# Performance work log

Hardware: AMD Instinct MI355X
Metric: run time of the kernel (lower is better)

## Reference

```python
import jax, jax.numpy as jnp
import numpy as np

N = 20000   # nodes
E = 240000  # edges (avg degree 12)
D = 128     # hidden_dim
H = 4       # heads
C = D // H  # head dim = 32
L = 3       # layers


def _ln(x, g, b):
    m = x.mean(-1, keepdims=True)
    v = ((x - m) ** 2).mean(-1, keepdims=True)
    return (x - m) / jnp.sqrt(v + 1e-5) * g + b


def setup_inputs() -> dict:
    key = jax.random.key(0)
    ks = iter(jax.random.split(key, 64))
    def w(shape, s=0.02):
        return jax.random.normal(next(ks), shape, jnp.float32) * s
    z = lambda shape: jnp.zeros(shape, jnp.float32)
    o = lambda shape: jnp.ones(shape, jnp.float32)
    inp = {
        'xyz': jax.random.normal(next(ks), (N, 3), jnp.float32) * 10.0,
        'attr': jax.random.uniform(next(ks), (N, 1), jnp.float32),
        'edge_index': jax.random.randint(next(ks), (2, E), 0, N, jnp.int32),
        # input encoder
        'enc_W': w((4, D)), 'enc_b': z((D,)), 'enc_g': o((D,)), 'enc_bb': z((D,)),
        # relative position MLP
        'pos_W1': w((3, D)), 'pos_b1': z((D,)), 'pos_g': o((D,)), 'pos_bb': z((D,)),
        'pos_W2': w((D, D)), 'pos_b2': z((D,)),
        # TransformerConv per-layer params (stacked over L)
        'Wq': w((L, D, D)), 'bq': z((L, D)),
        'Wk': w((L, D, D)), 'bk': z((L, D)),
        'Wv': w((L, D, D)), 'bv': z((L, D)),
        'We': w((L, D, D)),                 # lin_edge (no bias in PyG)
        'Wskip': w((L, D, D)), 'bskip': z((L, D)),
        'Wbeta': w((L, 3 * D, 1)),          # lin_beta (no bias)
        'ln1_g': o((L, D)), 'ln1_b': z((L, D)),
        'ln2_g': o((L, D)), 'ln2_b': z((L, D)),
        'fW1': w((L, D, 2 * D)), 'fb1': z((L, 2 * D)),
        'fW2': w((L, 2 * D, D)), 'fb2': z((L, D)),
        # heads
        'cls_W1': w((D, D // 2)), 'cls_b1': z((D // 2,)),
        'cls_W2': w((D // 2, 4)), 'cls_b2': z((4,)),
        'box_W1': w((D, D // 2)), 'box_b1': z((D // 2,)),
        'box_W2': w((D // 2, 7)), 'box_b2': z((7,)),
    }
    return inp


def reference(xyz, attr, edge_index, enc_W, enc_b, enc_g, enc_bb,
              pos_W1, pos_b1, pos_g, pos_bb, pos_W2, pos_b2,
              Wq, bq, Wk, bk, Wv, bv, We, Wskip, bskip, Wbeta,
              ln1_g, ln1_b, ln2_g, ln2_b, fW1, fb1, fW2, fb2,
              cls_W1, cls_b1, cls_W2, cls_b2, box_W1, box_b1, box_W2, box_b2):
    n = xyz.shape[0]
    src, dst = edge_index[0], edge_index[1]  # x_j = x[src], x_i = x[dst]; aggregate at dst
    inv_sqrt_c = 1.0 / float(np.sqrt(C))

    # input encoder: Linear -> LayerNorm -> ReLU
    x = jnp.concatenate([xyz, attr], axis=-1)
    x = jax.nn.relu(_ln(x @ enc_W + enc_b, enc_g, enc_bb))

    # relative position encoding per edge: i, j = edge_index; rel = xyz[j] - xyz[i]
    rel = xyz[dst] - xyz[src]
    e = jax.nn.relu(_ln(rel @ pos_W1 + pos_b1, pos_g, pos_bb)) @ pos_W2 + pos_b2  # [E, D]

    for l in range(L):
        # TransformerConv (beta=True, concat=True, edge_dim=D), eval mode (no dropout)
        q = (x @ Wq[l] + bq[l]).reshape(n, H, C)
        k = (x @ Wk[l] + bk[l]).reshape(n, H, C)
        v = (x @ Wv[l] + bv[l]).reshape(n, H, C)
        ee = (e @ We[l]).reshape(-1, H, C)          # [E, H, C]
        kj = k[src] + ee                             # edge-conditioned keys
        alpha = (q[dst] * kj).sum(-1) * inv_sqrt_c   # [E, H]
        amax = jax.ops.segment_max(alpha, dst, num_segments=n)
        ex = jnp.exp(alpha - amax[dst])
        den = jax.ops.segment_sum(ex, dst, num_segments=n)
        a = ex / den[dst]                            # scatter softmax over in-edges of dst
        msg = (v[src] + ee) * a[:, :, None]
        out = jax.ops.segment_sum(msg, dst, num_segments=n).reshape(n, D)
        # beta-gated skip
        r = x @ Wskip[l] + bskip[l]
        beta = jax.nn.sigmoid(jnp.concatenate([out, r, out - r], axis=-1) @ Wbeta[l])  # [N,1]
        out = beta * r + (1.0 - beta) * out
        # residual + LN + FFN + residual + LN
        x = _ln(out + x, ln1_g[l], ln1_b[l])
        h = jax.nn.gelu(x @ fW1[l] + fb1[l], approximate=False) @ fW2[l] + fb2[l]
        x = _ln(h + x, ln2_g[l], ln2_b[l])

    cls_logits = jax.nn.relu(x @ cls_W1 + cls_b1) @ cls_W2 + cls_b2  # [N, 4]
    box_pred = jax.nn.relu(x @ box_W1 + box_b1) @ box_W2 + box_b2    # [N, 7]
    return (cls_logits, box_pred)
```

## Files before the change

kernel.cpp:

```cpp
#include <hip/hip_runtime.h>
#include <hip/hip_bf16.h>
#include <math.h>

#define DD 128

typedef __attribute__((ext_vector_type(8))) short short8;
typedef __attribute__((ext_vector_type(4))) float f32x4;


__device__ __forceinline__ unsigned short f2b(float f) {
    unsigned u = __float_as_uint(f);
    return (unsigned short)((u + 0x7FFFu + ((u >> 16) & 1u)) >> 16);
}
__device__ __forceinline__ float b2f(unsigned short b) {
    return __uint_as_float(((unsigned)b) << 16);
}
__device__ __forceinline__ unsigned packbf(float a, float b) {
    return (unsigned)f2b(a) | ((unsigned)f2b(b) << 16);
}

__device__ __forceinline__ void redsum2_128(float& a, float& b) {
    #pragma unroll
    for (int off = 32; off > 0; off >>= 1) {
        a += __shfl_down(a, off);
        b += __shfl_down(b, off);
    }
    __shared__ float sa[2], sb[2];
    int w = threadIdx.x >> 6;
    if ((threadIdx.x & 63) == 0) { sa[w] = a; sb[w] = b; }
    __syncthreads();
    a = sa[0] + sa[1];
    b = sb[0] + sb[1];
    __syncthreads();
}


__global__ void packw12_kernel(const float* __restrict__ Wq, const float* __restrict__ Wk,
                               const float* __restrict__ Wv, const float* __restrict__ Ws,
                               unsigned* __restrict__ Wp) {
    int bid = blockIdx.x, y = blockIdx.y, d = threadIdx.x;
    int l = y >> 2, wt = y & 3;
    const float* W = (wt == 0 ? Wq : wt == 1 ? Wk : wt == 2 ? Wv : Ws) + (size_t)l * DD * DD;
    float w0 = W[(size_t)(2 * bid) * DD + d];
    float w1 = W[(size_t)(2 * bid + 1) * DD + d];
    Wp[y * 8192 + (((d << 6) + bid) ^ ((d & 7) << 2))] = packbf(w0, w1);
}

__global__ void wcombp_kernel(const float* __restrict__ W2, const float* __restrict__ b2,
                              const float* __restrict__ We, unsigned* __restrict__ Wp,
                              float* __restrict__ b2We) {
    int bid = blockIdx.x, y = blockIdx.y, d = threadIdx.x;
    const float* We_l = We + (size_t)y * DD * DD;
    __shared__ float sa0[DD], sa1[DD];
    if (bid < 64) { sa0[d] = W2[(2 * bid) * DD + d]; sa1[d] = W2[(2 * bid + 1) * DD + d]; }
    else          { sa0[d] = b2[d]; sa1[d] = 0.f; }
    __syncthreads();
    float acc0 = 0.f, acc1 = 0.f;
    #pragma unroll 8
    for (int kk = 0; kk < DD; ++kk) {
        float w = We_l[kk * DD + d];
        acc0 += sa0[kk] * w;
        acc1 += sa1[kk] * w;
    }
    if (bid < 64) Wp[y * 8192 + (((d << 6) + bid) ^ ((d & 7) << 2))] = packbf(acc0, acc1);
    else          b2We[y * DD + d] = acc0;
}

struct B4 { const float* b[4]; };

__global__ __launch_bounds__(256) void proj_kernel(
        const unsigned short* __restrict__ xb, const unsigned* __restrict__ Wp4, B4 bias,
        unsigned short* __restrict__ qkv, float* __restrict__ rbuf, int rowsN, int rtN,
        const float4* __restrict__ rel4, const float* __restrict__ pw,
        const float* __restrict__ bbp, const unsigned* __restrict__ Wpee,
        const float* __restrict__ biasee, unsigned short* __restrict__ eeout,
        int rowsE, int rtE) {
    __shared__ unsigned Bt[8192];
    __shared__ float sc[640];
    const int t = threadIdx.x;
    const int lane = t & 63, wid = t >> 6;
    const int kqo = (lane >> 4) * 8;

    if ((int)blockIdx.x < rtE) {
        const int rowBase = (int)blockIdx.x << 6;
        #pragma unroll
        for (int i = 0; i < 8; ++i)
            *(uint4*)&Bt[(i * 256 + t) * 4] = *(const uint4*)&Wpee[(i * 256 + t) * 4];
        for (int i = t; i < 640; i += 256)
            sc[i] = (i < 512) ? pw[i] : bbp[i - 512];
        int arow = rowBase + wid * 16 + (lane & 15);
        if (arow > rowsE - 1) arow = rowsE - 1;
        float4 rv = rel4[arow];
        __syncthreads();
        short8 a[4];
        #pragma unroll
        for (int kc = 0; kc < 4; ++kc) {
            union { short8 s; unsigned short u[8]; } cv;
            #pragma unroll
            for (int j = 0; j < 8; ++j) {
                int d = kc * 32 + kqo + j;
                float y = fmaf(rv.x, sc[d], fmaf(rv.y, sc[128 + d], fmaf(rv.z, sc[256 + d], sc[384 + d])));
                cv.u[j] = f2b(fmaxf(fmaf(y, rv.w, sc[512 + d]), 0.f));
            }
            a[kc] = cv.s;
        }
        f32x4 acc[8];
        #pragma unroll
        for (int i = 0; i < 8; ++i) acc[i] = (f32x4){0.f, 0.f, 0.f, 0.f};
        #pragma unroll
        for (int ng = 0; ng < 8; ++ng) {
            int col = ng * 16 + (lane & 15);
            #pragma unroll
            for (int kc = 0; kc < 4; ++kc) {
                int kidx = kc * 16 + (lane >> 4) * 4;
                const short8 b = *(const short8*)((const char*)Bt +
                        ((((col << 6) + kidx) ^ ((col & 7) << 2)) << 2));
                acc[ng] = __builtin_amdgcn_mfma_f32_16x16x32_bf16(a[kc], b, acc[ng], 0, 0, 0);
            }
        }
        __syncthreads();
        unsigned short* sb16 = (unsigned short*)Bt;
        #pragma unroll
        for (int ng = 0; ng < 8; ++ng) {
            int col = ng * 16 + (lane & 15);
            float bv = biasee[col];
            int cp = col >> 1, cb = col & 1;
            #pragma unroll
            for (int r = 0; r < 4; ++r) {
                int row = wid * 16 + (lane >> 4) * 4 + r;
                sb16[((row << 6) + (cp ^ ((row & 7) << 2))) * 2 + cb] = f2b(acc[ng][r] + bv);
            }
        }
        __syncthreads();
        unsigned* outw = (unsigned*)eeout;
        #pragma unroll
        for (int i = 0; i < 4; ++i) {
            int j = i * 1024 + t * 4;
            int row = j >> 6, cp = j & 63;
            uint4 v = *(const uint4*)&Bt[(row << 6) + (cp ^ ((row & 7) << 2))];
            int grow = rowBase + row;
            if (grow < rowsE) *(uint4*)&outw[(size_t)grow * 64 + cp] = v;
        }
    } else {
        int bidx = (int)blockIdx.x - rtE;
        const int y = bidx / rtN;
        const int rowBase = (bidx % rtN) << 6;
        const unsigned* Wp = Wp4 + y * 8192;
        #pragma unroll
        for (int i = 0; i < 8; ++i)
            *(uint4*)&Bt[(i * 256 + t) * 4] = *(const uint4*)&Wp[(i * 256 + t) * 4];
        int arow = rowBase + wid * 16 + (lane & 15);
        if (arow > rowsN - 1) arow = rowsN - 1;
        short8 a[4];
        #pragma unroll
        for (int kc = 0; kc < 4; ++kc)
            a[kc] = *(const short8*)(xb + (size_t)arow * DD + kc * 32 + kqo);
        __syncthreads();
        f32x4 acc[8];
        #pragma unroll
        for (int i = 0; i < 8; ++i) acc[i] = (f32x4){0.f, 0.f, 0.f, 0.f};
        #pragma unroll
        for (int ng = 0; ng < 8; ++ng) {
            int col = ng * 16 + (lane & 15);
            #pragma unroll
            for (int kc = 0; kc < 4; ++kc) {
                int kidx = kc * 16 + (lane >> 4) * 4;
                const short8 b = *(const short8*)((const char*)Bt +
                        ((((col << 6) + kidx) ^ ((col & 7) << 2)) << 2));
                acc[ng] = __builtin_amdgcn_mfma_f32_16x16x32_bf16(a[kc], b, acc[ng], 0, 0, 0);
            }
        }
        const float* bs = bias.b[y];
        if (y == 3) {
            #pragma unroll
            for (int ng = 0; ng < 8; ++ng) {
                int col = ng * 16 + (lane & 15);
                float bv = bs[col];
                #pragma unroll
                for (int r = 0; r < 4; ++r) {
                    int grow = rowBase + wid * 16 + (lane >> 4) * 4 + r;
                    if (grow < rowsN) rbuf[(size_t)grow * DD + col] = acc[ng][r] + bv;
                }
            }
            return;
        }
        __syncthreads();
        unsigned short* sb16 = (unsigned short*)Bt;
        #pragma unroll
        for (int ng = 0; ng < 8; ++ng) {
            int col = ng * 16 + (lane & 15);
            float bv = bs[col];
            int cp = col >> 1, cb = col & 1;
            #pragma unroll
            for (int r = 0; r < 4; ++r) {
                int row = wid * 16 + (lane >> 4) * 4 + r;
                sb16[((row << 6) + (cp ^ ((row & 7) << 2))) * 2 + cb] = f2b(acc[ng][r] + bv);
            }
        }
        __syncthreads();
        unsigned* outw = (unsigned*)qkv;
        #pragma unroll
        for (int i = 0; i < 4; ++i) {
            int j = i * 1024 + t * 4;
            int row = j >> 6, cp = j & 63;
            uint4 v = *(const uint4*)&Bt[(row << 6) + (cp ^ ((row & 7) << 2))];
            int grow = rowBase + row;
            if (grow < rowsN) *(uint4*)&outw[(size_t)grow * 192 + (y << 6) + cp] = v;
        }
    }
}

template <int ACT>
__global__ __launch_bounds__(256) void mgemm(
        const unsigned short* __restrict__ A, const float* __restrict__ W,
        const float* __restrict__ bias, unsigned short* __restrict__ out,
        int rows, int K, int Dout) {
    __shared__ unsigned Bt[8192];
    const int t = threadIdx.x;
    const int rowBase = blockIdx.x << 6;
    const int colBase = blockIdx.y << 7;
    const int lane = t & 63, wid = t >> 6;
    f32x4 acc[8];
    #pragma unroll
    for (int i = 0; i < 8; ++i) acc[i] = (f32x4){0.f, 0.f, 0.f, 0.f};
    int arow = rowBase + wid * 16 + (lane & 15);
    if (arow > rows - 1) arow = rows - 1;
    const int kqo = (lane >> 4) * 8;
    for (int k0 = 0; k0 < K; k0 += 128) {
        if (k0) __syncthreads();
        #pragma unroll 8
        for (int it = 0; it < 32; ++it) {
            int idx = it * 256 + t;
            int n = idx & 127, kp = idx >> 7;
            int krow = k0 + kp * 2;
            float w0 = W[(size_t)krow * Dout + colBase + n];
            float w1 = W[(size_t)(krow + 1) * Dout + colBase + n];
            Bt[((n << 6) + kp) ^ ((n & 7) << 2)] = packbf(w0, w1);
        }
        __syncthreads();
        short8 a[4];
        #pragma unroll
        for (int kc = 0; kc < 4; ++kc)
            a[kc] = *(const short8*)(A + (size_t)arow * K + k0 + kc * 32 + kqo);
        #pragma unroll
        for (int ng = 0; ng < 8; ++ng) {
            int col = ng * 16 + (lane & 15);
            #pragma unroll
            for (int kc = 0; kc < 4; ++kc) {
                int kidx = kc * 16 + (lane >> 4) * 4;
                const short8 b = *(const short8*)((const char*)Bt +
                        ((((col << 6) + kidx) ^ ((col & 7) << 2)) << 2));
                acc[ng] = __builtin_amdgcn_mfma_f32_16x16x32_bf16(a[kc], b, acc[ng], 0, 0, 0);
            }
        }
    }
    __syncthreads();
    unsigned short* sb16 = (unsigned short*)Bt;
    #pragma unroll
    for (int ng = 0; ng < 8; ++ng) {
        int col = ng * 16 + (lane & 15);
        float bv = bias[colBase + col];
        int cp = col >> 1, cb = col & 1;
        #pragma unroll
        for (int r = 0; r < 4; ++r) {
            int row = wid * 16 + (lane >> 4) * 4 + r;
            float val = acc[ng][r] + bv;
            if (ACT == 1) val = 0.5f * val * (1.f + erff(val * 0.70710678118654752f));
            else if (ACT == 2) val = fmaxf(val, 0.f);
            sb16[((row << 6) + (cp ^ ((row & 7) << 2))) * 2 + cb] = f2b(val);
        }
    }
    __syncthreads();
    unsigned* outw = (unsigned*)out;
    const int strideU = Dout >> 1, cbU = colBase >> 1;
    #pragma unroll
    for (int i = 0; i < 4; ++i) {
        int j = i * 1024 + t * 4;
        int row = j >> 6, cp = j & 63;
        uint4 v = *(const uint4*)&Bt[(row << 6) + (cp ^ ((row & 7) << 2))];
        int grow = rowBase + row;
        if (grow < rows) *(uint4*)&outw[(size_t)grow * strideU + cbU + cp] = v;
    }
}

__global__ __launch_bounds__(256) void ffn_fused(
        const unsigned short* __restrict__ xbin, const float* __restrict__ W1,
        const float* __restrict__ b1f, const float* __restrict__ W2,
        const float* __restrict__ b2f, const float* __restrict__ g,
        const float* __restrict__ bbn, float* __restrict__ x,
        unsigned short* __restrict__ xb, int rows) {
    __shared__ unsigned Bt[8192];
    __shared__ unsigned h1t[8192];
    const int t = threadIdx.x;
    const int rowBase = blockIdx.x << 6;
    const int lane = t & 63, wid = t >> 6;
    const int kqo = (lane >> 4) * 8;
    int arow = rowBase + wid * 16 + (lane & 15);
    if (arow > rows - 1) arow = rows - 1;

    short8 a[4];
    #pragma unroll
    for (int kc = 0; kc < 4; ++kc)
        a[kc] = *(const short8*)(xbin + (size_t)arow * DD + kc * 32 + kqo);

    unsigned short* h16 = (unsigned short*)h1t;
    for (int half = 0; half < 2; ++half) {
        if (half) __syncthreads();
        #pragma unroll 8
        for (int it = 0; it < 32; ++it) {
            int idx = it * 256 + t;
            int n = idx & 127, kp = idx >> 7;
            float w0 = W1[(size_t)(2 * kp) * 256 + half * 128 + n];
            float w1 = W1[(size_t)(2 * kp + 1) * 256 + half * 128 + n];
            Bt[((n << 6) + kp) ^ ((n & 7) << 2)] = packbf(w0, w1);
        }
        __syncthreads();
        f32x4 acc[8];
        #pragma unroll
        for (int i = 0; i < 8; ++i) acc[i] = (f32x4){0.f, 0.f, 0.f, 0.f};
        #pragma unroll
        for (int ng = 0; ng < 8; ++ng) {
            int col = ng * 16 + (lane & 15);
            #pragma unroll
            for (int kc = 0; kc < 4; ++kc) {
                int kidx = kc * 16 + (lane >> 4) * 4;
                const short8 b = *(const short8*)((const char*)Bt +
                        ((((col << 6) + kidx) ^ ((col & 7) << 2)) << 2));
                acc[ng] = __builtin_amdgcn_mfma_f32_16x16x32_bf16(a[kc], b, acc[ng], 0, 0, 0);
            }
        }
        #pragma unroll
        for (int ng = 0; ng < 8; ++ng) {
            int col = half * 128 + ng * 16 + (lane & 15);
            float bv = b1f[col];
            int cp = col >> 1, cb = col & 1;
            #pragma unroll
            for (int r = 0; r < 4; ++r) {
                int row = wid * 16 + (lane >> 4) * 4 + r;
                float val = acc[ng][r] + bv;
                val = 0.5f * val * (1.f + erff(val * 0.70710678118654752f));
                h16[((row << 7) + (cp ^ ((row & 7) << 2))) * 2 + cb] = f2b(val);
            }
        }
    }
    f32x4 accF[8];
    #pragma unroll
    for (int i = 0; i < 8; ++i) accF[i] = (f32x4){0.f, 0.f, 0.f, 0.f};
    const int lrow = wid * 16 + (lane & 15);
    for (int c = 0; c < 2; ++c) {
        __syncthreads();
        #pragma unroll 8
        for (int it = 0; it < 32; ++it) {
            int idx = it * 256 + t;
            int n = idx & 127, kp = idx >> 7;
            int krow = c * 128 + kp * 2;
            float w0 = W2[(size_t)krow * DD + n];
            float w1 = W2[(size_t)(krow + 1) * DD + n];
            Bt[((n << 6) + kp) ^ ((n & 7) << 2)] = packbf(w0, w1);
        }
        __syncthreads();
        short8 ah[4];
        #pragma unroll
        for (int kc = 0; kc < 4; ++kc) {
            int cp4 = c * 64 + kc * 16 + (lane >> 4) * 4;
            ah[kc] = *(const short8*)&h1t[(lrow << 7) + (cp4 ^ ((lrow & 7) << 2))];
        }
        #pragma unroll
        for (int ng = 0; ng < 8; ++ng) {
            int col = ng * 16 + (lane & 15);
            #pragma unroll
            for (int kc = 0; kc < 4; ++kc) {
                int kidx = kc * 16 + (lane >> 4) * 4;
                const short8 b = *(const short8*)((const char*)Bt +
                        ((((col << 6) + kidx) ^ ((col & 7) << 2)) << 2));
                accF[ng] = __builtin_amdgcn_mfma_f32_16x16x32_bf16(ah[kc], b, accF[ng], 0, 0, 0);
            }
        }
    }
    float tt[8][4];
    float rs[4] = {0.f, 0.f, 0.f, 0.f}, rs2[4] = {0.f, 0.f, 0.f, 0.f};
    #pragma unroll
    for (int ng = 0; ng < 8; ++ng) {
        int col = ng * 16 + (lane & 15);
        float bv = b2f[col];
        #pragma unroll
        for (int r = 0; r < 4; ++r) {
            int grow = rowBase + wid * 16 + (lane >> 4) * 4 + r;
            float xo = (grow < rows) ? x[(size_t)grow * DD + col] : 0.f;
            float v = accF[ng][r] + bv + xo;
            tt[ng][r] = v;
            rs[r] += v;
            rs2[r] += v * v;
        }
    }
    #pragma unroll
    for (int r = 0; r < 4; ++r) {
        #pragma unroll
        for (int m = 1; m < 16; m <<= 1) {
            rs[r] += __shfl_xor(rs[r], m);
            rs2[r] += __shfl_xor(rs2[r], m);
        }
    }
    __syncthreads();
    unsigned short* sb16 = (unsigned short*)Bt;
    #pragma unroll
    for (int ng = 0; ng < 8; ++ng) {
        int col = ng * 16 + (lane & 15);
        float gg = g[col], bbb = bbn[col];
        int cp = col >> 1, cb = col & 1;
        #pragma unroll
        for (int r = 0; r < 4; ++r) {
            int grow = rowBase + wid * 16 + (lane >> 4) * 4 + r;
            float mean = rs[r] * (1.f / DD);
            float var = rs2[r] * (1.f / DD) - mean * mean;
            float val = (tt[ng][r] - mean) * rsqrtf(var + 1e-5f) * gg + bbb;
            if (grow < rows) x[(size_t)grow * DD + col] = val;
            int row = wid * 16 + (lane >> 4) * 4 + r;
            sb16[((row << 6) + (cp ^ ((row & 7) << 2))) * 2 + cb] = f2b(val);
        }
    }
    __syncthreads();
    unsigned* outw = (unsigned*)xb;
    #pragma unroll
    for (int i = 0; i < 4; ++i) {
        int j = i * 1024 + t * 4;
        int row = j >> 6, cp = j & 63;
        uint4 v = *(const uint4*)&Bt[(row << 6) + (cp ^ ((row & 7) << 2))];
        int grow = rowBase + row;
        if (grow < rows) *(uint4*)&outw[(size_t)grow * 64 + cp] = v;
    }
}


__global__ void enc_kernel(const float* __restrict__ xyz, const float* __restrict__ attr,
                           const float* __restrict__ W, const float* __restrict__ b,
                           const float* __restrict__ g, const float* __restrict__ bb,
                           float* __restrict__ x, unsigned short* __restrict__ xb) {
    int i = blockIdx.x, d = threadIdx.x;
    __shared__ float sin4[4];
    if (d < 3) sin4[d] = xyz[i * 3 + d];
    if (d == 3) sin4[3] = attr[i];
    __syncthreads();
    float y = b[d];
    #pragma unroll
    for (int kk = 0; kk < 4; ++kk) y += sin4[kk] * W[kk * DD + d];
    float s = y, s2 = y * y;
    redsum2_128(s, s2);
    float mean = s * (1.0f / DD);
    float var = s2 * (1.0f / DD) - mean * mean;
    float xn = fmaxf((y - mean) * rsqrtf(var + 1e-5f) * g[d] + bb[d], 0.f);
    x[i * DD + d] = xn;
    xb[(size_t)i * DD + d] = f2b(xn);
}

__global__ void posprep_kernel(const float* __restrict__ W1, const float* __restrict__ b1,
                               const float* __restrict__ g, float* __restrict__ pw) {
    int d = threadIdx.x;
    float w0 = W1[d], w1 = W1[DD + d], w2 = W1[2 * DD + d], b = b1[d];
    float s0 = w0, s1 = w1;
    redsum2_128(s0, s1);
    float s2 = w2, s3 = b;
    redsum2_128(s2, s3);
    float c0 = w0 - s0 * (1.f / DD), c1 = w1 - s1 * (1.f / DD);
    float c2 = w2 - s2 * (1.f / DD), bc = b - s3 * (1.f / DD);
    float gd = g[d];
    pw[d] = c0 * gd; pw[DD + d] = c1 * gd; pw[2 * DD + d] = c2 * gd; pw[3 * DD + d] = bc * gd;
    float p0 = c0 * c0, p1 = c0 * c1; redsum2_128(p0, p1);
    float p2 = c0 * c2, p3 = c1 * c1; redsum2_128(p2, p3);
    float p4 = c1 * c2, p5 = c2 * c2; redsum2_128(p4, p5);
    float p6 = c0 * bc, p7 = c1 * bc; redsum2_128(p6, p7);
    float p8 = c2 * bc, p9 = bc * bc; redsum2_128(p8, p9);
    if (d == 0) {
        pw[512] = p0 * (1.f / DD); pw[513] = p1 * (1.f / DD); pw[514] = p2 * (1.f / DD);
        pw[515] = p3 * (1.f / DD); pw[516] = p4 * (1.f / DD); pw[517] = p5 * (1.f / DD);
        pw[518] = p6 * (1.f / DD); pw[519] = p7 * (1.f / DD); pw[520] = p8 * (1.f / DD);
        pw[521] = p9 * (1.f / DD);
    }
}


__global__ void hist_kernel(const int* __restrict__ ei, int* __restrict__ deg, int E) {
    int e = blockIdx.x * blockDim.x + threadIdx.x;
    if (e < E) atomicAdd(&deg[ei[E + e]], 1);
}

__global__ void scan_kernel(const int* __restrict__ deg, int* __restrict__ ptr, int n) {
    __shared__ int partial[1024];
    int t = threadIdx.x;
    int CH = (n + 1023) >> 10;
    int beg = t * CH;
    int end = beg + CH; if (end > n) end = n;
    int s = 0;
    for (int i = beg; i < end; ++i) s += deg[i];
    partial[t] = s;
    __syncthreads();
    for (int off = 1; off < 1024; off <<= 1) {
        int add = (t >= off) ? partial[t - off] : 0;
        __syncthreads();
        partial[t] += add;
        __syncthreads();
    }
    int base = (t == 0) ? 0 : partial[t - 1];
    for (int i = beg; i < end; ++i) {
        ptr[i] = base;
        base += deg[i];
    }
    if (end == n && beg < n) ptr[n] = base;
}

__global__ void scatter_kernel(const int* __restrict__ ei, const float* __restrict__ xyz,
                               const float* __restrict__ pw, const int* __restrict__ ptr,
                               int* __restrict__ cur, int* __restrict__ cs_src,
                               float4* __restrict__ rel4, int E) {
    int e = blockIdx.x * blockDim.x + threadIdx.x;
    if (e >= E) return;
    int srcn = ei[e], dstn = ei[E + e];
    int p = atomicAdd(&cur[dstn], 1);
    int slot = ptr[dstn] + p;
    cs_src[slot] = srcn;
    float r0 = xyz[dstn * 3]     - xyz[srcn * 3];
    float r1 = xyz[dstn * 3 + 1] - xyz[srcn * 3 + 1];
    float r2 = xyz[dstn * 3 + 2] - xyz[srcn * 3 + 2];
    float var = pw[512] * r0 * r0 + pw[515] * r1 * r1 + pw[517] * r2 * r2
              + 2.f * (pw[513] * r0 * r1 + pw[514] * r0 * r2 + pw[516] * r1 * r2)
              + 2.f * (pw[518] * r0 + pw[519] * r1 + pw[520] * r2) + pw[521];
    rel4[slot] = make_float4(r0, r1, r2, rsqrtf(var + 1e-5f));
}

__global__ __launch_bounds__(256) void aggc_kernel(
        const unsigned* __restrict__ qkv, const unsigned* __restrict__ ee,
        const int* __restrict__ ptr, const int* __restrict__ cs_src,
        const float* __restrict__ r, const float* __restrict__ Wb,
        const float* __restrict__ g1, const float* __restrict__ b1,
        float* __restrict__ x, unsigned* __restrict__ xbw, int N) {
    const int wave = threadIdx.x >> 6;
    const int lane = threadIdx.x & 63;
    const int node = ((int)blockIdx.x << 1) + (wave >> 1);
    const int half = wave & 1;
    __shared__ float sS[4];
    __shared__ float sA0[4][64];
    __shared__ float sA1[4][64];

    float s = 0.f, a0 = 0.f, a1 = 0.f;
    float q0 = 0.f, q1 = 0.f;
    int beg = 0, end = 0;
    if (node < N) {
        unsigned qp = qkv[(size_t)node * 192 + lane];
        q0 = b2f((unsigned short)qp);
        q1 = b2f((unsigned short)(qp >> 16));
        beg = ptr[node];
        end = ptr[node + 1];
    }
    int idx = beg + half;
    unsigned epN = 0, kpN = 0, vpN = 0;
    if (idx < end) {
        int j = cs_src[idx];
        epN = __builtin_nontemporal_load(&ee[(size_t)idx * 64 + lane]);
        kpN = qkv[(size_t)j * 192 + 64 + lane];
        vpN = qkv[(size_t)j * 192 + 128 + lane];
    }
    for (; idx < end; idx += 2) {
        unsigned ep = epN, kp = kpN, vp = vpN;
        int nidx = idx + 2;
        if (nidx < end) {
            int jn = cs_src[nidx];
            epN = __builtin_nontemporal_load(&ee[(size_t)nidx * 64 + lane]);
            kpN = qkv[(size_t)jn * 192 + 64 + lane];
            vpN = qkv[(size_t)jn * 192 + 128 + lane];
        }
        float e0 = b2f((unsigned short)ep), e1 = b2f((unsigned short)(ep >> 16));
        float kj0 = b2f((unsigned short)kp) + e0;
        float kj1 = b2f((unsigned short)(kp >> 16)) + e1;
        float p = q0 * kj0 + q1 * kj1;
        p += __shfl_xor(p, 1); p += __shfl_xor(p, 2);
        p += __shfl_xor(p, 4); p += __shfl_xor(p, 8);
        float w = __expf(p * 0.17677669529663687f);
        s += w;
        a0 += (b2f((unsigned short)vp) + e0) * w;
        a1 += (b2f((unsigned short)(vp >> 16)) + e1) * w;
    }
    sS[wave] = s;
    sA0[wave][lane] = a0;
    sA1[wave][lane] = a1;
    __syncthreads();
    if (half != 0 || node >= N) return;
    s  = sS[wave] + sS[wave + 1];
    a0 = sA0[wave][lane] + sA0[wave + 1][lane];
    a1 = sA1[wave][lane] + sA1[wave + 1][lane];

    float inv_s = (s > 0.f) ? 1.f / s : 0.f;
    float od0 = a0 * inv_s, od1 = a1 * inv_s;
    float2 rd = *(const float2*)&r[(size_t)node * DD + lane * 2];
    float2 wb0 = *(const float2*)&Wb[lane * 2];
    float2 wb1 = *(const float2*)&Wb[DD + lane * 2];
    float2 wb2 = *(const float2*)&Wb[2 * DD + lane * 2];
    float part = od0 * wb0.x + rd.x * wb1.x + (od0 - rd.x) * wb2.x
               + od1 * wb0.y + rd.y * wb1.y + (od1 - rd.y) * wb2.y;
    #pragma unroll
    for (int m = 1; m < 64; m <<= 1) part += __shfl_xor(part, m);
    float beta = 1.f / (1.f + __expf(-part));
    float2 xo = *(const float2*)&x[(size_t)node * DD + lane * 2];
    float t0 = beta * rd.x + (1.f - beta) * od0 + xo.x;
    float t1 = beta * rd.y + (1.f - beta) * od1 + xo.y;
    float ss = t0 + t1, ss2 = t0 * t0 + t1 * t1;
    #pragma unroll
    for (int m = 1; m < 64; m <<= 1) { ss += __shfl_xor(ss, m); ss2 += __shfl_xor(ss2, m); }
    float mean = ss * (1.f / DD);
    float var = ss2 * (1.f / DD) - mean * mean;
    float inv = rsqrtf(var + 1e-5f);
    float2 gg = *(const float2*)&g1[lane * 2];
    float2 bbv = *(const float2*)&b1[lane * 2];
    float2 res;
    res.x = (t0 - mean) * inv * gg.x + bbv.x;
    res.y = (t1 - mean) * inv * gg.y + bbv.y;
    *(float2*)&x[(size_t)node * DD + lane * 2] = res;
    xbw[(size_t)node * 64 + lane] = packbf(res.x, res.y);
}


__global__ void headprep_kernel(const float* __restrict__ cW1, const float* __restrict__ cb1,
                                const float* __restrict__ bW1, const float* __restrict__ bb1,
                                float* __restrict__ W1cat, float* __restrict__ b1cat) {
    int kk = blockIdx.x, d = threadIdx.x;
    W1cat[kk * DD + d] = (d < 64) ? cW1[kk * 64 + d] : bW1[kk * 64 + (d - 64)];
    if (kk == 0) b1cat[d] = (d < 64) ? cb1[d] : bb1[d - 64];
}

__global__ __launch_bounds__(256) void heads2_kernel(
        const unsigned* __restrict__ hh, const float* __restrict__ cW2,
        const float* __restrict__ cb2, const float* __restrict__ bW2,
        const float* __restrict__ bb2, float* __restrict__ outc,
        float* __restrict__ outb, int N) {
    int node = (blockIdx.x << 2) + (threadIdx.x >> 6);
    if (node >= N) return;
    const int lane = threadIdx.x & 63;
    unsigned hp = hh[(size_t)node * 64 + lane];
    float h0 = b2f((unsigned short)hp), h1 = b2f((unsigned short)(hp >> 16));
    bool isCls = lane < 32;
    int dd = isCls ? 2 * lane : 2 * lane - 128 + 64;
    float c[4], bx[7];
    #pragma unroll
    for (int j = 0; j < 4; ++j)
        c[j] = isCls ? h0 * cW2[dd * 4 + j] + h1 * cW2[(dd + 1) * 4 + j] : 0.f;
    #pragma unroll
    for (int j = 0; j < 7; ++j)
        bx[j] = isCls ? 0.f : h0 * bW2[dd * 7 + j] + h1 * bW2[(dd + 1) * 7 + j];
    #pragma unroll
    for (int m = 1; m < 32; m <<= 1) {
        #pragma unroll
        for (int j = 0; j < 4; ++j) c[j] += __shfl_xor(c[j], m);
        #pragma unroll
        for (int j = 0; j < 7; ++j) bx[j] += __shfl_xor(bx[j], m);
    }
    if (lane == 0) {
        #pragma unroll
        for (int j = 0; j < 4; ++j) outc[(size_t)node * 4 + j] = c[j] + cb2[j];
    } else if (lane == 32) {
        #pragma unroll
        for (int j = 0; j < 7; ++j) outb[(size_t)node * 7 + j] = bx[j] + bb2[j];
    }
}

extern "C" void kernel_launch(void* const* d_in, const int* in_sizes, int n_in,
                              void* d_out, int out_size, void* d_ws, size_t ws_size,
                              hipStream_t stream) {
    const float* xyz   = (const float*)d_in[0];
    const float* attr  = (const float*)d_in[1];
    const int*   ei    = (const int*)d_in[2];
    const float* encW  = (const float*)d_in[3];
    const float* encb  = (const float*)d_in[4];
    const float* encg  = (const float*)d_in[5];
    const float* encbb = (const float*)d_in[6];
    const float* posW1 = (const float*)d_in[7];
    const float* posb1 = (const float*)d_in[8];
    const float* posg  = (const float*)d_in[9];
    const float* posbb = (const float*)d_in[10];
    const float* posW2 = (const float*)d_in[11];
    const float* posb2 = (const float*)d_in[12];
    const float* Wq    = (const float*)d_in[13];
    const float* bq    = (const float*)d_in[14];
    const float* Wk    = (const float*)d_in[15];
    const float* bk    = (const float*)d_in[16];
    const float* Wv    = (const float*)d_in[17];
    const float* bv    = (const float*)d_in[18];
    const float* We    = (const float*)d_in[19];
    const float* Wskip = (const float*)d_in[20];
    const float* bskip = (const float*)d_in[21];
    const float* Wbeta = (const float*)d_in[22];
    const float* ln1g  = (const float*)d_in[23];
    const float* ln1b  = (const float*)d_in[24];
    const float* ln2g  = (const float*)d_in[25];
    const float* ln2b  = (const float*)d_in[26];
    const float* fW1   = (const float*)d_in[27];
    const float* fb1   = (const float*)d_in[28];
    const float* fW2   = (const float*)d_in[29];
    const float* fb2   = (const float*)d_in[30];
    const float* cW1   = (const float*)d_in[31];
    const float* cb1   = (const float*)d_in[32];
    const float* cW2   = (const float*)d_in[33];
    const float* cb2   = (const float*)d_in[34];
    const float* bW1   = (const float*)d_in[35];
    const float* bb1   = (const float*)d_in[36];
    const float* bW2   = (const float*)d_in[37];
    const float* bb2   = (const float*)d_in[38];

    const int N = in_sizes[0] / 3;
    const int E = in_sizes[2] / 2;

    size_t off = 0;
    auto alloc = [&](size_t nelem) {
        char* p = (char*)d_ws + off;
        off += nelem * sizeof(float);
        return (float*)p;
    };
    float* x     = alloc((size_t)N * DD);
    unsigned short* qkv = (unsigned short*)alloc((size_t)N * 192);
    float* r     = alloc((size_t)N * DD);
    unsigned short* h1 = (unsigned short*)alloc((size_t)N * 128);
    unsigned short* xb = (unsigned short*)alloc((size_t)N * 64);
    float4* rel4 = (float4*)alloc((size_t)E * 4);
    unsigned short* eeb = (unsigned short*)alloc((size_t)E * 64);
    unsigned* W2Wep = (unsigned*)alloc(3 * 8192);
    float* b2We  = alloc(3 * DD);
    unsigned* Wp12 = (unsigned*)alloc(12 * 8192);
    float* pw    = alloc(544);
    float* W1cat = alloc(DD * DD);
    float* b1cat = alloc(DD);
    int* deg     = (int*)alloc(N);
    int* ptr     = (int*)alloc(N + 1);
    int* cur     = (int*)alloc(N);
    int* cs_src  = (int*)alloc(E);

    const int rtN = (N + 63) / 64;
    const int rtE = (E + 63) / 64;

    enc_kernel<<<N, DD, 0, stream>>>(xyz, attr, encW, encb, encg, encbb, x, xb);
    hipMemsetAsync(deg, 0, N * sizeof(int), stream);
    hipMemsetAsync(cur, 0, N * sizeof(int), stream);
    hist_kernel<<<(E + 255) / 256, 256, 0, stream>>>(ei, deg, E);
    scan_kernel<<<1, 1024, 0, stream>>>(deg, ptr, N);
    posprep_kernel<<<1, DD, 0, stream>>>(posW1, posb1, posg, pw);
    scatter_kernel<<<(E + 255) / 256, 256, 0, stream>>>(ei, xyz, pw, ptr, cur, cs_src, rel4, E);
    wcombp_kernel<<<dim3(65, 3), DD, 0, stream>>>(posW2, posb2, We, W2Wep, b2We);
    packw12_kernel<<<dim3(64, 12), DD, 0, stream>>>(Wq, Wk, Wv, Wskip, Wp12);
    headprep_kernel<<<DD, DD, 0, stream>>>(cW1, cb1, bW1, bb1, W1cat, b1cat);

    for (int l = 0; l < 3; ++l) {
        const float* Wb_l = Wbeta + (size_t)l * 3 * DD;
        const float* fW1_l = fW1 + (size_t)l * DD * 256;
        const float* fW2_l = fW2 + (size_t)l * 256 * DD;
        B4 bs;
        bs.b[0] = bq + l * DD; bs.b[1] = bk + l * DD;
        bs.b[2] = bv + l * DD; bs.b[3] = bskip + l * DD;

        proj_kernel<<<rtE + 4 * rtN, 256, 0, stream>>>(
            xb, Wp12 + (size_t)l * 4 * 8192, bs, qkv, r, N, rtN,
            rel4, pw, posbb, W2Wep + l * 8192, b2We + l * DD, eeb, E, rtE);

        aggc_kernel<<<(N + 1) / 2, 256, 0, stream>>>((const unsigned*)qkv, (const unsigned*)eeb,
                                                     ptr, cs_src, r, Wb_l,
                                                     ln1g + l * DD, ln1b + l * DD,
                                                     x, (unsigned*)xb, N);

        ffn_fused<<<rtN, 256, 0, stream>>>(xb, fW1_l, fb1 + l * 256, fW2_l, fb2 + l * DD,
                                           ln2g + l * DD, ln2b + l * DD, x, xb, N);
    }

    float* outc  = (float*)d_out;
    float* outbx = (float*)d_out + (size_t)N * 4;
    mgemm<2><<<dim3(rtN, 1), 256, 0, stream>>>(xb, W1cat, b1cat, h1, N, DD, DD);
    heads2_kernel<<<(N + 3) / 4, 256, 0, stream>>>((const unsigned*)h1, cW2, cb2, bW2, bb2,
                                                   outc, outbx, N);
}
```

Measured before the change: 428.7 us.

## Interleave K and V in qkv buffer and use one node per aggregation block

The projection kernel now writes K and V interleaved per 32-bit pair, so the aggregation kernel fetches both with a single 8-byte gather per source node instead of two separate 4-byte loads. The aggregation kernel is also reorganised to process one node per 256-thread block, with four waves striding over the in-edges instead of two, and combines their partials through shared memory. This is meant to cut gather transactions and add memory-level parallelism for high-degree nodes. The cost is scattered 4-byte stores in the projection epilogue and twice as many blocks, many of them idle-heavy for low-degree nodes.

```diff
diff --git a/kernel.cpp b/kernel.cpp
--- a/kernel.cpp
+++ b/kernel.cpp
@@ -199,13 +199,28 @@
         }
         __syncthreads();
         unsigned* outw = (unsigned*)qkv;
-        #pragma unroll
-        for (int i = 0; i < 4; ++i) {
-            int j = i * 1024 + t * 4;
-            int row = j >> 6, cp = j & 63;
-            uint4 v = *(const uint4*)&Bt[(row << 6) + (cp ^ ((row & 7) << 2))];
-            int grow = rowBase + row;
-            if (grow < rowsN) *(uint4*)&outw[(size_t)grow * 192 + (y << 6) + cp] = v;
+        if (y == 0) {
+            #pragma unroll
+            for (int i = 0; i < 4; ++i) {
+                int j = i * 1024 + t * 4;
+                int row = j >> 6, cp = j & 63;
+                uint4 v = *(const uint4*)&Bt[(row << 6) + (cp ^ ((row & 7) << 2))];
+                int grow = rowBase + row;
+                if (grow < rowsN) *(uint4*)&outw[(size_t)grow * 192 + cp] = v;
+            }
+        } else {
+            const int sub = y - 1;
+            #pragma unroll
+            for (int i = 0; i < 4; ++i) {
+                int j = i * 1024 + t * 4;
+                int row = j >> 6, cp = j & 63;
+                uint4 v = *(const uint4*)&Bt[(row << 6) + (cp ^ ((row & 7) << 2))];
+                int grow = rowBase + row;
+                if (grow < rowsN) {
+                    unsigned* base = &outw[(size_t)grow * 192 + 64 + 2 * cp + sub];
+                    base[0] = v.x; base[2] = v.y; base[4] = v.z; base[6] = v.w;
+                }
+            }
         }
     }
 }
@@ -535,58 +550,51 @@
         float* __restrict__ x, unsigned* __restrict__ xbw, int N) {
     const int wave = threadIdx.x >> 6;
     const int lane = threadIdx.x & 63;
-    const int node = ((int)blockIdx.x << 1) + (wave >> 1);
-    const int half = wave & 1;
+    const int node = blockIdx.x;
     __shared__ float sS[4];
     __shared__ float sA0[4][64];
     __shared__ float sA1[4][64];
 
+    unsigned qp = qkv[(size_t)node * 192 + lane];
+    float q0 = b2f((unsigned short)qp), q1 = b2f((unsigned short)(qp >> 16));
+    int beg = ptr[node], end = ptr[node + 1];
     float s = 0.f, a0 = 0.f, a1 = 0.f;
-    float q0 = 0.f, q1 = 0.f;
-    int beg = 0, end = 0;
-    if (node < N) {
-        unsigned qp = qkv[(size_t)node * 192 + lane];
-        q0 = b2f((unsigned short)qp);
-        q1 = b2f((unsigned short)(qp >> 16));
-        beg = ptr[node];
-        end = ptr[node + 1];
-    }
-    int idx = beg + half;
-    unsigned epN = 0, kpN = 0, vpN = 0;
+    int idx = beg + wave;
+    unsigned epN = 0;
+    uint2 kvN = make_uint2(0u, 0u);
     if (idx < end) {
         int j = cs_src[idx];
         epN = __builtin_nontemporal_load(&ee[(size_t)idx * 64 + lane]);
-        kpN = qkv[(size_t)j * 192 + 64 + lane];
-        vpN = qkv[(size_t)j * 192 + 128 + lane];
-    }
-    for (; idx < end; idx += 2) {
-        unsigned ep = epN, kp = kpN, vp = vpN;
-        int nidx = idx + 2;
+        kvN = *(const uint2*)&qkv[(size_t)j * 192 + 64 + 2 * lane];
+    }
+    for (; idx < end; idx += 4) {
+        unsigned ep = epN;
+        uint2 kv = kvN;
+        int nidx = idx + 4;
         if (nidx < end) {
             int jn = cs_src[nidx];
             epN = __builtin_nontemporal_load(&ee[(size_t)nidx * 64 + lane]);
-            kpN = qkv[(size_t)jn * 192 + 64 + lane];
-            vpN = qkv[(size_t)jn * 192 + 128 + lane];
+            kvN = *(const uint2*)&qkv[(size_t)jn * 192 + 64 + 2 * lane];
         }
         float e0 = b2f((unsigned short)ep), e1 = b2f((unsigned short)(ep >> 16));
-        float kj0 = b2f((unsigned short)kp) + e0;
-        float kj1 = b2f((unsigned short)(kp >> 16)) + e1;
+        float kj0 = b2f((unsigned short)kv.x) + e0;
+        float kj1 = b2f((unsigned short)(kv.x >> 16)) + e1;
         float p = q0 * kj0 + q1 * kj1;
         p += __shfl_xor(p, 1); p += __shfl_xor(p, 2);
         p += __shfl_xor(p, 4); p += __shfl_xor(p, 8);
         float w = __expf(p * 0.17677669529663687f);
         s += w;
-        a0 += (b2f((unsigned short)vp) + e0) * w;
-        a1 += (b2f((unsigned short)(vp >> 16)) + e1) * w;
+        a0 += (b2f((unsigned short)kv.y) + e0) * w;
+        a1 += (b2f((unsigned short)(kv.y >> 16)) + e1) * w;
     }
     sS[wave] = s;
     sA0[wave][lane] = a0;
     sA1[wave][lane] = a1;
     __syncthreads();
-    if (half != 0 || node >= N) return;
-    s  = sS[wave] + sS[wave + 1];
-    a0 = sA0[wave][lane] + sA0[wave + 1][lane];
-    a1 = sA1[wave][lane] + sA1[wave + 1][lane];
+    if (wave != 0) return;
+    s  = sS[0] + sS[1] + sS[2] + sS[3];
+    a0 = sA0[0][lane] + sA0[1][lane] + sA0[2][lane] + sA0[3][lane];
+    a1 = sA1[0][lane] + sA1[1][lane] + sA1[2][lane] + sA1[3][lane];
 
     float inv_s = (s > 0.f) ? 1.f / s : 0.f;
     float od0 = a0 * inv_s, od1 = a1 * inv_s;
@@ -757,10 +765,10 @@
             xb, Wp12 + (size_t)l * 4 * 8192, bs, qkv, r, N, rtN,
             rel4, pw, posbb, W2Wep + l * 8192, b2We + l * DD, eeb, E, rtE);
 
-        aggc_kernel<<<(N + 1) / 2, 256, 0, stream>>>((const unsigned*)qkv, (const unsigned*)eeb,
-                                                     ptr, cs_src, r, Wb_l,
-                                                     ln1g + l * DD, ln1b + l * DD,
-                                                     x, (unsigned*)xb, N);
+        aggc_kernel<<<N, 256, 0, stream>>>((const unsigned*)qkv, (const unsigned*)eeb,
+                                           ptr, cs_src, r, Wb_l,
+                                           ln1g + l * DD, ln1b + l * DD,
+                                           x, (unsigned*)xb, N);
 
         ffn_fused<<<rtN, 256, 0, stream>>>(xb, fW1_l, fb1 + l * 256, fW2_l, fb2 + l * DD,
                                            ln2g + l * DD, ln2b + l * DD, x, xb, N);
```

Result: slower. 441.8 us (+3.1%).
